# Performance work log

Measured on AMD Instinct MI355X. Metric: run time of the kernel, lower is better.

Reference implementation:

```python
import jax, jax.numpy as jnp
import numpy as np

DIM = 64
NUM_GRAPHS = 256  # B: number of graphs in the batch (static)


def setup_inputs() -> dict:
    key = jax.random.key(0)
    ks = jax.random.split(key, 16)
    N, E = 8000, 40000

    def p(k, shape, s=0.1):
        return jax.random.normal(k, shape, jnp.float32) * s

    return dict(
        x=jax.random.normal(ks[0], (N, 21), jnp.float32),
        edge_attr=jax.random.uniform(ks[1], (E, 16), jnp.float32),
        edge_index=jax.random.randint(ks[2], (2, E), 0, N, jnp.int32),
        batch=jnp.sort(jax.random.randint(ks[3], (N,), 0, NUM_GRAPHS, jnp.int32)),
        lin0_w=p(ks[4], (DIM, 21)), lin0_b=jnp.zeros((DIM,), jnp.float32),
        nn_w1=p(ks[5], (128, 16)), nn_b1=jnp.zeros((128,), jnp.float32),
        nn_w2=p(ks[6], (DIM * DIM, 128), 0.02), nn_b2=jnp.zeros((DIM * DIM,), jnp.float32),
        conv_root=p(ks[7], (DIM, DIM)), conv_bias=jnp.zeros((DIM,), jnp.float32),
        gru_w_ih=p(ks[8], (3 * DIM, DIM)), gru_w_hh=p(ks[9], (3 * DIM, DIM)),
        gru_b_ih=jnp.zeros((3 * DIM,), jnp.float32), gru_b_hh=jnp.zeros((3 * DIM,), jnp.float32),
        lstm_w_ih=p(ks[10], (4 * DIM, 2 * DIM)), lstm_w_hh=p(ks[11], (4 * DIM, DIM)),
        lstm_b_ih=jnp.zeros((4 * DIM,), jnp.float32), lstm_b_hh=jnp.zeros((4 * DIM,), jnp.float32),
        lin1_w=p(ks[12], (DIM, 2 * DIM)), lin1_b=jnp.zeros((DIM,), jnp.float32),
        lin2_w=p(ks[13], (1, DIM)), lin2_b=jnp.zeros((1,), jnp.float32),
    )


def reference(x, edge_attr, edge_index, batch,
              lin0_w, lin0_b, nn_w1, nn_b1, nn_w2, nn_b2,
              conv_root, conv_bias, gru_w_ih, gru_w_hh, gru_b_ih, gru_b_hh,
              lstm_w_ih, lstm_w_hh, lstm_b_ih, lstm_b_hh,
              lin1_w, lin1_b, lin2_w, lin2_b):
    N = x.shape[0]
    src, dst = edge_index[0], edge_index[1]

    out = jax.nn.relu(x @ lin0_w.T + lin0_b)           # [N, 64]
    h = out

    # edge-conditioned weights (same every iteration): [E, 64, 64]
    e_h = jax.nn.relu(edge_attr @ nn_w1.T + nn_b1)
    w_e = (e_h @ nn_w2.T + nn_b2).reshape(-1, DIM, DIM)

    deg = jax.ops.segment_sum(jnp.ones_like(src, jnp.float32), dst, num_segments=N)
    deg = jnp.maximum(deg, 1.0)[:, None]

    for _ in range(3):
        # NNConv: gather + per-edge matmul + scatter-mean + root/bias
        msg = jnp.einsum('ei,eio->eo', out[src], w_e)  # [E, 64]
        agg = jax.ops.segment_sum(msg, dst, num_segments=N) / deg
        m = jax.nn.relu(agg + out @ conv_root + conv_bias)
        # GRU cell (seq_len = 1), torch gate order r, z, n
        gi = m @ gru_w_ih.T + gru_b_ih
        gh = h @ gru_w_hh.T + gru_b_hh
        ir, iz, i_n = jnp.split(gi, 3, axis=-1)
        hr, hz, h_n = jnp.split(gh, 3, axis=-1)
        r = jax.nn.sigmoid(ir + hr)
        z = jax.nn.sigmoid(iz + hz)
        n = jnp.tanh(i_n + r * h_n)
        h = (1.0 - z) * n + z * h
        out = h

    # Set2Set pooling, 3 processing steps
    B = NUM_GRAPHS
    q_star = jnp.zeros((B, 2 * DIM), x.dtype)
    hs = jnp.zeros((B, DIM), x.dtype)
    cs = jnp.zeros((B, DIM), x.dtype)
    for _ in range(3):
        gates = q_star @ lstm_w_ih.T + lstm_b_ih + hs @ lstm_w_hh.T + lstm_b_hh
        gi_, gf_, gg_, go_ = jnp.split(gates, 4, axis=-1)  # torch gate order i,f,g,o
        cs = jax.nn.sigmoid(gf_) * cs + jax.nn.sigmoid(gi_) * jnp.tanh(gg_)
        hs = jax.nn.sigmoid(go_) * jnp.tanh(cs)
        q = hs                                             # [B, 64]
        e = jnp.sum(out * q[batch], axis=-1)               # [N]
        mmax = jax.ops.segment_max(e, batch, num_segments=B)
        ex = jnp.exp(e - mmax[batch])
        s = jax.ops.segment_sum(ex, batch, num_segments=B)
        a = ex / s[batch]
        r_read = jax.ops.segment_sum(a[:, None] * out, batch, num_segments=B)
        q_star = jnp.concatenate([q, r_read], axis=-1)     # [B, 128]

    y = jax.nn.relu(q_star @ lin1_w.T + lin1_b)
    y = y @ lin2_w.T + lin2_b
    return y.reshape(-1)
```

## Files before the change

### kernel.cpp

```cpp
#include <hip/hip_runtime.h>
#include <math.h>

#define NN 8000
#define NE 40000
#define NGB 256
#define SK 8192
#define KSPLIT 16

typedef unsigned int u32;
typedef unsigned short u16;
typedef __attribute__((ext_vector_type(8))) short short8v;
typedef __attribute__((ext_vector_type(4))) float float4v;
typedef __attribute__((ext_vector_type(4))) unsigned int uint4v;

__device__ __forceinline__ float sigmoidf_(float x) { return 1.f / (1.f + expf(-x)); }

__device__ __forceinline__ u32 bf16_rne(float f) {
    u32 x = __builtin_bit_cast(u32, f);
    return (x + 0x7FFFu + ((x >> 16) & 1u)) >> 16;
}

__device__ __forceinline__ uint4v pack_bf8(const float v[8]) {
    u32 h[8];
#pragma unroll
    for (int j = 0; j < 8; ++j) h[j] = bf16_rne(v[j]);
    return (uint4v){ h[0] | (h[1] << 16), h[2] | (h[3] << 16),
                     h[4] | (h[5] << 16), h[6] | (h[7] << 16) };
}

__device__ __forceinline__ void pack8(const float* p, float scale, short8v& ah, short8v& al) {
    float v[8];
#pragma unroll
    for (int j = 0; j < 8; ++j) v[j] = p[j];
    u32 hu[8], lu[8];
#pragma unroll
    for (int j = 0; j < 8; ++j) {
        float s = v[j] * scale;
        hu[j] = bf16_rne(s);
        float fh = __builtin_bit_cast(float, hu[j] << 16);
        lu[j] = bf16_rne(s - fh);
    }
    uint4v hset = { hu[0] | (hu[1] << 16), hu[2] | (hu[3] << 16),
                    hu[4] | (hu[5] << 16), hu[6] | (hu[7] << 16) };
    uint4v lset = { lu[0] | (lu[1] << 16), lu[2] | (lu[3] << 16),
                    lu[4] | (lu[5] << 16), lu[6] | (lu[7] << 16) };
    ah = __builtin_bit_cast(short8v, hset);
    al = __builtin_bit_cast(short8v, lset);
}


__global__ void k_lin0(const float* __restrict__ x, const float* __restrict__ w,
                       const float* __restrict__ b, float* __restrict__ out) {
    __shared__ float xr[21];
    int n = blockIdx.x, t = threadIdx.x;
    if (t < 21) xr[t] = x[n * 21 + t];
    __syncthreads();
    float s = b[t];
#pragma unroll
    for (int c = 0; c < 21; ++c) s += xr[c] * w[t * 21 + c];
    out[n * 64 + t] = fmaxf(s, 0.f);
}

__global__ void k_eh(const float* __restrict__ ea, const float* __restrict__ w1,
                     const float* __restrict__ b1, float* __restrict__ e_h) {
    __shared__ float a[2][16];
    int t = threadIdx.x;
    int e0 = blockIdx.x * 2;
    if (t < 32) a[t >> 4][t & 15] = ea[(e0 + (t >> 4)) * 16 + (t & 15)];
    __syncthreads();
    int sub = t >> 7, j = t & 127;
    float s = b1[j];
#pragma unroll
    for (int c = 0; c < 16; ++c) s += a[sub][c] * w1[j * 16 + c];
    e_h[(size_t)(e0 + sub) * 128 + j] = fmaxf(s, 0.f);
}

__global__ void k_prep(const float* __restrict__ nn_w2, const float* __restrict__ conv_root,
                       const float* __restrict__ nn_b2, const float* __restrict__ w_ih,
                       const float* __restrict__ w_hh,
                       u16* __restrict__ Whi, u16* __restrict__ Wlo,
                       u16* __restrict__ Bmh, u16* __restrict__ Bml,
                       u16* __restrict__ Bih_h, u16* __restrict__ Bih_l,
                       u16* __restrict__ Bhh_h, u16* __restrict__ Bhh_l) {
    int idx = blockIdx.x * 256 + threadIdx.x;
    if (idx < 524288) {
        int o = idx >> 13, kap = idx & 8191;
        int i = kap >> 7, k = kap & 127;
        float v = nn_w2[(size_t)((i << 6) + o) * 128 + k];
        u32 h = bf16_rne(v);
        float fh = __builtin_bit_cast(float, h << 16);
        u32 l = bf16_rne(v - fh);
        int pos = ((kap >> 3) * 64 + o) * 8 + (kap & 7);
        Whi[pos] = (u16)h; Wlo[pos] = (u16)l;
    } else if (idx < 524288 + 8192) {
        int i2 = idx - 524288;
        int k = i2 >> 6, o = i2 & 63;
        float v = (k < 64) ? nn_b2[k * 64 + o] : conv_root[(k - 64) * 64 + o];
        u32 h = bf16_rne(v);
        float fh = __builtin_bit_cast(float, h << 16);
        u32 l = bf16_rne(v - fh);
        int pos = ((k >> 3) * 64 + o) * 8 + (k & 7);
        Bmh[pos] = (u16)h; Bml[pos] = (u16)l;
    } else if (idx < 524288 + 8192 + 24576) {
        int i3 = idx - 524288 - 8192;
        int half = i3 >= 12288;
        int i2 = i3 - half * 12288;
        int o = i2 % 192, k = i2 / 192;
        float v = half ? w_hh[o * 64 + k] : w_ih[o * 64 + k];
        u32 h = bf16_rne(v);
        float fh = __builtin_bit_cast(float, h << 16);
        u32 l = bf16_rne(v - fh);
        int pos = ((k >> 3) * 192 + o) * 8 + (k & 7);
        if (half) { Bhh_h[pos] = (u16)h; Bhh_l[pos] = (u16)l; }
        else      { Bih_h[pos] = (u16)h; Bih_l[pos] = (u16)l; }
    }
}

__global__ void k_deg(const int* __restrict__ dst, int* __restrict__ degi) {
    int e = blockIdx.x * blockDim.x + threadIdx.x;
    if (e < NE) atomicAdd(&degi[dst[e]], 1);
}

__global__ __launch_bounds__(1024) void k_scan(
    const int* __restrict__ degi, int* __restrict__ rowptr,
    int* __restrict__ cursor, float* __restrict__ degf) {
    __shared__ int tsum[1024];
    int t = threadIdx.x;
    int base = t * 8;
    int v[8];
    int s = 0;
#pragma unroll
    for (int j = 0; j < 8; ++j) {
        int i = base + j;
        v[j] = (i < NN) ? degi[i] : 0;
        s += v[j];
    }
    tsum[t] = s;
    __syncthreads();
    for (int off = 1; off < 1024; off <<= 1) {
        int add = (t >= off) ? tsum[t - off] : 0;
        __syncthreads();
        tsum[t] += add;
        __syncthreads();
    }
    int exc = (t == 0) ? 0 : tsum[t - 1];
#pragma unroll
    for (int j = 0; j < 8; ++j) {
        int i = base + j;
        if (i < NN) {
            rowptr[i] = exc; cursor[i] = exc;
            degf[i] = (float)(v[j] > 1 ? v[j] : 1);
            exc += v[j];
        }
    }
    if (t == 1023) rowptr[NN] = tsum[1023];
}

__global__ void k_fill(const int* __restrict__ dst, int* __restrict__ cursor,
                       int* __restrict__ elist) {
    int e = blockIdx.x * blockDim.x + threadIdx.x;
    if (e < NE) { int p = atomicAdd(&cursor[dst[e]], 1); elist[p] = e; }
}

__global__ void k_gstart(const int* __restrict__ batch, int* __restrict__ gstart) {
    int g = blockIdx.x * blockDim.x + threadIdx.x;
    if (g > NGB) return;
    int lo = 0, hi = NN;
    while (lo < hi) { int mid = (lo + hi) >> 1; if (batch[mid] < g) lo = mid + 1; else hi = mid; }
    gstart[g] = lo;
}

__global__ __launch_bounds__(256) void k_sbuild(
    const float* __restrict__ out, const float* __restrict__ e_h,
    const int* __restrict__ src, const int* __restrict__ rowptr,
    const int* __restrict__ elist, u16* __restrict__ S_bf,
    float* __restrict__ Osum, int base) {
    int t = threadIdx.x;
    int n = base + blockIdx.x;
    int ig = t >> 4;
    int k8 = t & 15;
    int lane = t & 63;
    float acc[4][8];
#pragma unroll
    for (int j = 0; j < 4; ++j)
#pragma unroll
        for (int c = 0; c < 8; ++c) acc[j][c] = 0.f;
    float osum = 0.f;
    int r0 = rowptr[n], r1 = rowptr[n + 1];
    const float4* out4 = (const float4*)out;
    const float4* eh4p = (const float4*)e_h;
    for (int idx = r0; idx < r1; ++idx) {
        int e = elist[idx];
        int sn = src[e];
        float4 e0 = eh4p[(size_t)e * 32 + k8 * 2];
        float4 e1 = eh4p[(size_t)e * 32 + k8 * 2 + 1];
        float ehv[8] = {e0.x, e0.y, e0.z, e0.w, e1.x, e1.y, e1.z, e1.w};
        float4 f = out4[sn * 16 + ig];
        float fv[4] = {f.x, f.y, f.z, f.w};
#pragma unroll
        for (int j = 0; j < 4; ++j)
#pragma unroll
            for (int c = 0; c < 8; ++c) acc[j][c] += fv[j] * ehv[c];
        if (t < 64) osum += out[(size_t)sn * 64 + lane];
    }
    uint4v* S4 = (uint4v*)S_bf;
    size_t rb = (size_t)blockIdx.x * (SK / 8);
#pragma unroll
    for (int j = 0; j < 4; ++j)
        S4[rb + (size_t)(ig * 4 + j) * 16 + k8] = pack_bf8(acc[j]);
    if (t < 64) Osum[(size_t)n * 64 + lane] = osum;
}

__global__ __launch_bounds__(64) void k_gemm(
    const u16* __restrict__ S_bf, const u16* __restrict__ Whi,
    const u16* __restrict__ Wlo, float* __restrict__ P, int base) {
    int lane = threadIdx.x;
    int lrow = lane & 15, lkg = lane >> 4;
    int m0 = blockIdx.x * 32;
    int ks = blockIdx.y;
    int kbase = ks * (SK / KSPLIT);
    float4v acc[2][4];
#pragma unroll
    for (int ms = 0; ms < 2; ++ms)
#pragma unroll
        for (int nt = 0; nt < 4; ++nt) acc[ms][nt] = (float4v){0.f, 0.f, 0.f, 0.f};
    const short8v* bhv = (const short8v*)Whi;
    const short8v* blv = (const short8v*)Wlo;
    const u16* ar0 = S_bf + (size_t)(m0 + lrow) * SK + kbase + lkg * 8;
    const u16* ar1 = ar0 + (size_t)16 * SK;
    int kc0 = (kbase >> 3) + lkg;

#pragma unroll 4
    for (int kk = 0; kk < SK / KSPLIT / 32; ++kk) {
        short8v ah0 = *(const short8v*)(ar0 + kk * 32);
        short8v ah1 = *(const short8v*)(ar1 + kk * 32);
        int bo = (kc0 + kk * 4) * 64 + lrow;
        short8v bh[4], bl[4];
#pragma unroll
        for (int nt = 0; nt < 4; ++nt) { bh[nt] = bhv[bo + nt * 16]; bl[nt] = blv[bo + nt * 16]; }
#pragma unroll
        for (int nt = 0; nt < 4; ++nt) {
            acc[0][nt] = __builtin_amdgcn_mfma_f32_16x16x32_bf16(ah0, bh[nt], acc[0][nt], 0, 0, 0);
            acc[0][nt] = __builtin_amdgcn_mfma_f32_16x16x32_bf16(ah0, bl[nt], acc[0][nt], 0, 0, 0);
            acc[1][nt] = __builtin_amdgcn_mfma_f32_16x16x32_bf16(ah1, bh[nt], acc[1][nt], 0, 0, 0);
            acc[1][nt] = __builtin_amdgcn_mfma_f32_16x16x32_bf16(ah1, bl[nt], acc[1][nt], 0, 0, 0);
        }
    }
    int gbase = base + m0;
#pragma unroll
    for (int ms = 0; ms < 2; ++ms)
#pragma unroll
        for (int nt = 0; nt < 4; ++nt)
#pragma unroll
            for (int jj = 0; jj < 4; ++jj) {
                int row = ms * 16 + lkg * 4 + jj;
                int o = nt * 16 + lrow;
                P[((size_t)ks * NN + gbase + row) * 64 + o] = acc[ms][nt][jj];
            }
}

__global__ __launch_bounds__(64) void k_node(
    float* __restrict__ out, const float* __restrict__ P,
    const float* __restrict__ Osum, const float* __restrict__ degf,
    const u16* __restrict__ Bmh, const u16* __restrict__ Bml,
    const u16* __restrict__ Bih_h, const u16* __restrict__ Bih_l,
    const u16* __restrict__ Bhh_h, const u16* __restrict__ Bhh_l,
    const float* __restrict__ conv_bias,
    const float* __restrict__ gb_ih, const float* __restrict__ gb_hh) {
    __shared__ float lds[16][68];
    int lane = threadIdx.x;
    int lrow = lane & 15, lkg = lane >> 4;
    int n0 = blockIdx.x * 16;
    int arow = n0 + lrow;

    {
        const float4* P4 = (const float4*)P;
        float4 ps[4];
#pragma unroll
        for (int c = 0; c < 4; ++c) ps[c] = make_float4(0.f, 0.f, 0.f, 0.f);
        for (int p = 0; p < KSPLIT; ++p) {
#pragma unroll
            for (int c = 0; c < 4; ++c) {
                float4 v = P4[(size_t)p * (NN * 16) + (size_t)arow * 16 + lkg * 4 + c];
                ps[c].x += v.x; ps[c].y += v.y; ps[c].z += v.z; ps[c].w += v.w;
            }
        }
#pragma unroll
        for (int c = 0; c < 4; ++c)
            *(float4*)&lds[lrow][lkg * 16 + c * 4] = ps[c];
    }
    __syncthreads();

    float invd = 1.f / degf[arow];
    float4v acc[4];
#pragma unroll
    for (int nt = 0; nt < 4; ++nt) acc[nt] = (float4v){0.f, 0.f, 0.f, 0.f};
    const short8v* bhv = (const short8v*)Bmh;
    const short8v* blv = (const short8v*)Bml;
#pragma unroll
    for (int s = 0; s < 4; ++s) {
        short8v ah, al;
        if (s < 2) pack8(&Osum[(size_t)arow * 64 + s * 32 + lkg * 8], invd, ah, al);
        else       pack8(&out[(size_t)arow * 64 + (s - 2) * 32 + lkg * 8], 1.f, ah, al);
        int kc = s * 4 + lkg;
#pragma unroll
        for (int nt = 0; nt < 4; ++nt) {
            short8v bh = bhv[kc * 64 + nt * 16 + lrow];
            short8v bl = blv[kc * 64 + nt * 16 + lrow];
            acc[nt] = __builtin_amdgcn_mfma_f32_16x16x32_bf16(ah, bh, acc[nt], 0, 0, 0);
            acc[nt] = __builtin_amdgcn_mfma_f32_16x16x32_bf16(al, bh, acc[nt], 0, 0, 0);
            acc[nt] = __builtin_amdgcn_mfma_f32_16x16x32_bf16(ah, bl, acc[nt], 0, 0, 0);
        }
    }
    float invd2[4];
#pragma unroll
    for (int jj = 0; jj < 4; ++jj) invd2[jj] = 1.f / degf[n0 + lkg * 4 + jj];
    float mval[4][4];
#pragma unroll
    for (int nt = 0; nt < 4; ++nt) {
        int o = nt * 16 + lrow;
        float cb = conv_bias[o];
#pragma unroll
        for (int jj = 0; jj < 4; ++jj)
            mval[nt][jj] = fmaxf(acc[nt][jj] + lds[lkg * 4 + jj][o] * invd2[jj] + cb, 0.f);
    }
    __syncthreads();
#pragma unroll
    for (int nt = 0; nt < 4; ++nt)
#pragma unroll
        for (int jj = 0; jj < 4; ++jj)
            lds[lkg * 4 + jj][nt * 16 + lrow] = mval[nt][jj];
    __syncthreads();

    float4v ai[12], ah_[12];
#pragma unroll
    for (int nt = 0; nt < 12; ++nt) { ai[nt] = (float4v){0.f, 0.f, 0.f, 0.f}; ah_[nt] = (float4v){0.f, 0.f, 0.f, 0.f}; }
    const short8v* bih_h = (const short8v*)Bih_h;
    const short8v* bih_l = (const short8v*)Bih_l;
    const short8v* bhh_h = (const short8v*)Bhh_h;
    const short8v* bhh_l = (const short8v*)Bhh_l;
#pragma unroll
    for (int s = 0; s < 2; ++s) {
        short8v mh, ml, hh, hl;
        pack8(&lds[lrow][s * 32 + lkg * 8], 1.f, mh, ml);
        pack8(&out[(size_t)arow * 64 + s * 32 + lkg * 8], 1.f, hh, hl);
        int kc = s * 4 + lkg;
#pragma unroll
        for (int nt = 0; nt < 12; ++nt) {
            int bo = kc * 192 + nt * 16 + lrow;
            short8v b1 = bih_h[bo], b2 = bih_l[bo];
            ai[nt] = __builtin_amdgcn_mfma_f32_16x16x32_bf16(mh, b1, ai[nt], 0, 0, 0);
            ai[nt] = __builtin_amdgcn_mfma_f32_16x16x32_bf16(ml, b1, ai[nt], 0, 0, 0);
            ai[nt] = __builtin_amdgcn_mfma_f32_16x16x32_bf16(mh, b2, ai[nt], 0, 0, 0);
            short8v b3 = bhh_h[bo], b4 = bhh_l[bo];
            ah_[nt] = __builtin_amdgcn_mfma_f32_16x16x32_bf16(hh, b3, ah_[nt], 0, 0, 0);
            ah_[nt] = __builtin_amdgcn_mfma_f32_16x16x32_bf16(hl, b3, ah_[nt], 0, 0, 0);
            ah_[nt] = __builtin_amdgcn_mfma_f32_16x16x32_bf16(hh, b4, ah_[nt], 0, 0, 0);
        }
    }
#pragma unroll
    for (int nt = 0; nt < 4; ++nt) {
        int o = nt * 16 + lrow;
        float bi0 = gb_ih[o], bi1 = gb_ih[64 + o], bi2 = gb_ih[128 + o];
        float bh0 = gb_hh[o], bh1 = gb_hh[64 + o], bh2 = gb_hh[128 + o];
#pragma unroll
        for (int jj = 0; jj < 4; ++jj) {
            int row = n0 + lkg * 4 + jj;
            float ir = ai[nt][jj] + bi0,  hr = ah_[nt][jj] + bh0;
            float iz = ai[nt + 4][jj] + bi1, hz = ah_[nt + 4][jj] + bh1;
            float in_ = ai[nt + 8][jj] + bi2, hn = ah_[nt + 8][jj] + bh2;
            float r = sigmoidf_(ir + hr);
            float z = sigmoidf_(iz + hz);
            float nv = tanhf(in_ + r * hn);
            float ho = out[(size_t)row * 64 + o];
            out[(size_t)row * 64 + o] = (1.f - z) * nv + z * ho;
        }
    }
}

__global__ __launch_bounds__(256) void k_s2s(
    const float* __restrict__ out, const int* __restrict__ gstart,
    const float* __restrict__ lw_ih, const float* __restrict__ lw_hh,
    const float* __restrict__ lb_ih, const float* __restrict__ lb_hh,
    const float* __restrict__ lin1_w, const float* __restrict__ lin1_b,
    const float* __restrict__ lin2_w, const float* __restrict__ lin2_b,
    float* __restrict__ yout) {
    __shared__ float qs[128], hsL[64], csL[64], gates[256];
    __shared__ float pv[384];
    __shared__ float red[4][64];
    __shared__ float sswv[4], mmaxw[4];
    int g = blockIdx.x, t = threadIdx.x, wv = t >> 6, lane = t & 63;
    int s0 = gstart[g], s1 = gstart[g + 1];
    if (t < 128) qs[t] = 0.f;
    if (t < 64) { hsL[t] = 0.f; csL[t] = 0.f; }
    __syncthreads();
    for (int st = 0; st < 3; ++st) {
        float s = lb_ih[t] + lb_hh[t];
        const float4* wi = (const float4*)&lw_ih[t * 128];
#pragma unroll
        for (int i = 0; i < 32; ++i) {
            float4 a = wi[i];
            s += qs[i * 4] * a.x + qs[i * 4 + 1] * a.y + qs[i * 4 + 2] * a.z + qs[i * 4 + 3] * a.w;
        }
        const float4* wh = (const float4*)&lw_hh[t * 64];
#pragma unroll
        for (int i = 0; i < 16; ++i) {
            float4 a = wh[i];
            s += hsL[i * 4] * a.x + hsL[i * 4 + 1] * a.y + hsL[i * 4 + 2] * a.z + hsL[i * 4 + 3] * a.w;
        }
        gates[t] = s;
        __syncthreads();
        if (t < 64) {
            float ig = sigmoidf_(gates[t]);
            float fg = sigmoidf_(gates[64 + t]);
            float gg = tanhf(gates[128 + t]);
            float og = sigmoidf_(gates[192 + t]);
            float c = fg * csL[t] + ig * gg;
            csL[t] = c;
            hsL[t] = og * tanhf(c);
        }
        __syncthreads();
        float wmax = -1e30f;
        for (int i = s0 + wv; i < s1; i += 4) {
            float p = out[(size_t)i * 64 + lane] * hsL[lane];
#pragma unroll
            for (int off = 32; off >= 1; off >>= 1) p += __shfl_xor(p, off);
            if (lane == 0) pv[i - s0] = p;
            wmax = fmaxf(wmax, p);
        }
        if (lane == 0) mmaxw[wv] = wmax;
        __syncthreads();
        float mmax = fmaxf(fmaxf(mmaxw[0], mmaxw[1]), fmaxf(mmaxw[2], mmaxw[3]));
        float ssum = 0.f, racc = 0.f;
        for (int i = s0 + wv; i < s1; i += 4) {
            float w = expf(pv[i - s0] - mmax);
            ssum += w;
            racc += w * out[(size_t)i * 64 + lane];
        }
        red[wv][lane] = racc;
        if (lane == 0) sswv[wv] = ssum;
        __syncthreads();
        if (t < 64) {
            float rt = red[0][t] + red[1][t] + red[2][t] + red[3][t];
            float stot = sswv[0] + sswv[1] + sswv[2] + sswv[3];
            qs[t] = hsL[t];
            qs[64 + t] = (s1 > s0) ? rt / stot : 0.f;
        }
        __syncthreads();
    }
    if (t < 64) {
        float s = lin1_b[t];
        const float4* w1 = (const float4*)&lin1_w[t * 128];
#pragma unroll
        for (int i = 0; i < 32; ++i) {
            float4 a = w1[i];
            s += qs[i * 4] * a.x + qs[i * 4 + 1] * a.y + qs[i * 4 + 2] * a.z + qs[i * 4 + 3] * a.w;
        }
        s = fmaxf(s, 0.f) * lin2_w[t];
#pragma unroll
        for (int off = 32; off >= 1; off >>= 1) s += __shfl_xor(s, off);
        if (t == 0) yout[g] = s + lin2_b[0];
    }
}

extern "C" void kernel_launch(void* const* d_in, const int* in_sizes, int n_in,
                              void* d_out, int out_size, void* d_ws, size_t ws_size,
                              hipStream_t stream) {
    (void)in_sizes; (void)n_in; (void)out_size;
    const float* x        = (const float*)d_in[0];
    const float* eattr    = (const float*)d_in[1];
    const int*   ei       = (const int*)d_in[2];
    const int*   batch    = (const int*)d_in[3];
    const float* lin0_w   = (const float*)d_in[4];
    const float* lin0_b   = (const float*)d_in[5];
    const float* nn_w1    = (const float*)d_in[6];
    const float* nn_b1    = (const float*)d_in[7];
    const float* nn_w2    = (const float*)d_in[8];
    const float* nn_b2    = (const float*)d_in[9];
    const float* conv_root= (const float*)d_in[10];
    const float* conv_bias= (const float*)d_in[11];
    const float* gw_ih    = (const float*)d_in[12];
    const float* gw_hh    = (const float*)d_in[13];
    const float* gb_ih    = (const float*)d_in[14];
    const float* gb_hh    = (const float*)d_in[15];
    const float* lw_ih    = (const float*)d_in[16];
    const float* lw_hh    = (const float*)d_in[17];
    const float* lb_ih    = (const float*)d_in[18];
    const float* lb_hh    = (const float*)d_in[19];
    const float* lin1_w   = (const float*)d_in[20];
    const float* lin1_b   = (const float*)d_in[21];
    const float* lin2_w   = (const float*)d_in[22];
    const float* lin2_b   = (const float*)d_in[23];
    const int* src = ei;
    const int* dst = ei + NE;

    char* w = (char*)d_ws;
    auto alloc = [&](size_t bytes) { char* p = w; w += (bytes + 255) & ~(size_t)255; return p; };
    float* out    = (float*)alloc((size_t)NN * 64 * 4);
    float* e_h    = (float*)alloc((size_t)NE * 128 * 4);
    u16*   Whi    = (u16*)alloc((size_t)64 * SK * 2);
    u16*   Wlo    = (u16*)alloc((size_t)64 * SK * 2);
    float* P      = (float*)alloc((size_t)KSPLIT * NN * 64 * 4);
    float* Osum   = (float*)alloc((size_t)NN * 64 * 4);
    u16*   Bmh    = (u16*)alloc((size_t)8192 * 2);
    u16*   Bml    = (u16*)alloc((size_t)8192 * 2);
    u16*   Bih_h  = (u16*)alloc((size_t)12288 * 2);
    u16*   Bih_l  = (u16*)alloc((size_t)12288 * 2);
    u16*   Bhh_h  = (u16*)alloc((size_t)12288 * 2);
    u16*   Bhh_l  = (u16*)alloc((size_t)12288 * 2);
    float* degf   = (float*)alloc((size_t)NN * 4);
    int*   degi   = (int*)alloc((size_t)NN * 4);
    int*   rowptr = (int*)alloc((size_t)(NN + 1) * 4);
    int*   cursor = (int*)alloc((size_t)(NN + 1) * 4);
    int*   elist  = (int*)alloc((size_t)NE * 4);
    int*   gstart = (int*)alloc((size_t)(NGB + 1) * 4);
    size_t used = (size_t)(w - (char*)d_ws);
    size_t avail = ws_size > used ? ws_size - used : 0;
    size_t maxrows = avail / ((size_t)SK * 2);
    int chunkN = maxrows > (size_t)NN ? NN : (int)maxrows;
    chunkN = (chunkN / 64) * 64;
    if (chunkN < 64) chunkN = 64;
    u16* S_bf = (u16*)w;

    hipMemsetAsync(degi, 0, (size_t)NN * 4, stream);

    k_lin0<<<NN, 64, 0, stream>>>(x, lin0_w, lin0_b, out);
    k_eh<<<NE / 2, 256, 0, stream>>>(eattr, nn_w1, nn_b1, e_h);
    k_prep<<<2176, 256, 0, stream>>>(nn_w2, conv_root, nn_b2, gw_ih, gw_hh,
                                     Whi, Wlo, Bmh, Bml, Bih_h, Bih_l, Bhh_h, Bhh_l);
    k_deg<<<(NE + 255) / 256, 256, 0, stream>>>(dst, degi);
    k_scan<<<1, 1024, 0, stream>>>(degi, rowptr, cursor, degf);
    k_fill<<<(NE + 255) / 256, 256, 0, stream>>>(dst, cursor, elist);
    k_gstart<<<5, 64, 0, stream>>>(batch, gstart);

    for (int it = 0; it < 3; ++it) {
        for (int cb = 0; cb < NN; cb += chunkN) {
            int cn = (NN - cb) < chunkN ? (NN - cb) : chunkN;
            k_sbuild<<<cn, 256, 0, stream>>>(out, e_h, src, rowptr, elist, S_bf, Osum, cb);
            k_gemm<<<dim3(cn / 32, KSPLIT), 64, 0, stream>>>(S_bf, Whi, Wlo, P, cb);
        }
        k_node<<<NN / 16, 64, 0, stream>>>(out, P, Osum, degf, Bmh, Bml,
                                           Bih_h, Bih_l, Bhh_h, Bhh_l,
                                           conv_bias, gb_ih, gb_hh);
    }

    k_s2s<<<NGB, 256, 0, stream>>>(out, gstart, lw_ih, lw_hh, lb_ih, lb_hh,
                                   lin1_w, lin1_b, lin2_w, lin2_b, (float*)d_out);
}
```

Before: 384.3 us.

## Fuse setup kernels and replace split-K partial buffer with atomic accumulation

Merges lin0, edge MLP, weight prep and graph-start search into one setup launch. Replaces the KSPLIT partial-product buffer and its reduction in k_node with float atomicAdd into a single Psum buffer, which k_sbuild zeroes. The GEMM blocks now hold two waves each. This is meant to cut launch count and the write and read traffic of the 16-way partial buffer, at the cost of atomic contention and non-deterministic summation order.

```diff
diff --git a/kernel.cpp b/kernel.cpp
--- a/kernel.cpp
+++ b/kernel.cpp
@@ -48,42 +48,44 @@
     al = __builtin_bit_cast(short8v, lset);
 }
 
-
-__global__ void k_lin0(const float* __restrict__ x, const float* __restrict__ w,
-                       const float* __restrict__ b, float* __restrict__ out) {
-    __shared__ float xr[21];
-    int n = blockIdx.x, t = threadIdx.x;
-    if (t < 21) xr[t] = x[n * 21 + t];
-    __syncthreads();
-    float s = b[t];
-#pragma unroll
-    for (int c = 0; c < 21; ++c) s += xr[c] * w[t * 21 + c];
-    out[n * 64 + t] = fmaxf(s, 0.f);
-}
-
-__global__ void k_eh(const float* __restrict__ ea, const float* __restrict__ w1,
-                     const float* __restrict__ b1, float* __restrict__ e_h) {
-    __shared__ float a[2][16];
-    int t = threadIdx.x;
-    int e0 = blockIdx.x * 2;
-    if (t < 32) a[t >> 4][t & 15] = ea[(e0 + (t >> 4)) * 16 + (t & 15)];
-    __syncthreads();
-    int sub = t >> 7, j = t & 127;
-    float s = b1[j];
-#pragma unroll
-    for (int c = 0; c < 16; ++c) s += a[sub][c] * w1[j * 16 + c];
-    e_h[(size_t)(e0 + sub) * 128 + j] = fmaxf(s, 0.f);
-}
-
-__global__ void k_prep(const float* __restrict__ nn_w2, const float* __restrict__ conv_root,
-                       const float* __restrict__ nn_b2, const float* __restrict__ w_ih,
-                       const float* __restrict__ w_hh,
-                       u16* __restrict__ Whi, u16* __restrict__ Wlo,
-                       u16* __restrict__ Bmh, u16* __restrict__ Bml,
-                       u16* __restrict__ Bih_h, u16* __restrict__ Bih_l,
-                       u16* __restrict__ Bhh_h, u16* __restrict__ Bhh_l) {
+#define SETUP_LIN0 (NN * 64)
+#define SETUP_EH   (NE * 128)
+#define SETUP_W2   (64 * SK)
+#define SETUP_MW   8192
+#define SETUP_GB   24576
+__global__ void k_setup(const float* __restrict__ x, const float* __restrict__ lin0_w,
+                        const float* __restrict__ lin0_b,
+                        const float* __restrict__ ea, const float* __restrict__ nn_w1,
+                        const float* __restrict__ nn_b1,
+                        const float* __restrict__ nn_w2, const float* __restrict__ conv_root,
+                        const float* __restrict__ nn_b2, const float* __restrict__ gw_ih,
+                        const float* __restrict__ gw_hh, const int* __restrict__ batch,
+                        float* __restrict__ out, float* __restrict__ e_h,
+                        u16* __restrict__ Whi, u16* __restrict__ Wlo,
+                        u16* __restrict__ Bmh, u16* __restrict__ Bml,
+                        u16* __restrict__ Bih_h, u16* __restrict__ Bih_l,
+                        u16* __restrict__ Bhh_h, u16* __restrict__ Bhh_l,
+                        int* __restrict__ gstart) {
     int idx = blockIdx.x * 256 + threadIdx.x;
-    if (idx < 524288) {
+    if (idx < SETUP_LIN0) {
+        int n = idx >> 6, o = idx & 63;
+        float s = lin0_b[o];
+#pragma unroll
+        for (int c = 0; c < 21; ++c) s += x[n * 21 + c] * lin0_w[o * 21 + c];
+        out[idx] = fmaxf(s, 0.f);
+        return;
+    }
+    idx -= SETUP_LIN0;
+    if (idx < SETUP_EH) {
+        int e = idx >> 7, j = idx & 127;
+        float s = nn_b1[j];
+#pragma unroll
+        for (int c = 0; c < 16; ++c) s += ea[e * 16 + c] * nn_w1[j * 16 + c];
+        e_h[idx] = fmaxf(s, 0.f);
+        return;
+    }
+    idx -= SETUP_EH;
+    if (idx < SETUP_W2) {
         int o = idx >> 13, kap = idx & 8191;
         int i = kap >> 7, k = kap & 127;
         float v = nn_w2[(size_t)((i << 6) + o) * 128 + k];
@@ -92,29 +94,42 @@
         u32 l = bf16_rne(v - fh);
         int pos = ((kap >> 3) * 64 + o) * 8 + (kap & 7);
         Whi[pos] = (u16)h; Wlo[pos] = (u16)l;
-    } else if (idx < 524288 + 8192) {
-        int i2 = idx - 524288;
-        int k = i2 >> 6, o = i2 & 63;
+        return;
+    }
+    idx -= SETUP_W2;
+    if (idx < SETUP_MW) {
+        int k = idx >> 6, o = idx & 63;
         float v = (k < 64) ? nn_b2[k * 64 + o] : conv_root[(k - 64) * 64 + o];
         u32 h = bf16_rne(v);
         float fh = __builtin_bit_cast(float, h << 16);
         u32 l = bf16_rne(v - fh);
         int pos = ((k >> 3) * 64 + o) * 8 + (k & 7);
         Bmh[pos] = (u16)h; Bml[pos] = (u16)l;
-    } else if (idx < 524288 + 8192 + 24576) {
-        int i3 = idx - 524288 - 8192;
-        int half = i3 >= 12288;
-        int i2 = i3 - half * 12288;
+        return;
+    }
+    idx -= SETUP_MW;
+    if (idx < SETUP_GB) {
+        int half = idx >= 12288;
+        int i2 = idx - half * 12288;
         int o = i2 % 192, k = i2 / 192;
-        float v = half ? w_hh[o * 64 + k] : w_ih[o * 64 + k];
+        float v = half ? gw_hh[o * 64 + k] : gw_ih[o * 64 + k];
         u32 h = bf16_rne(v);
         float fh = __builtin_bit_cast(float, h << 16);
         u32 l = bf16_rne(v - fh);
         int pos = ((k >> 3) * 192 + o) * 8 + (k & 7);
         if (half) { Bhh_h[pos] = (u16)h; Bhh_l[pos] = (u16)l; }
         else      { Bih_h[pos] = (u16)h; Bih_l[pos] = (u16)l; }
-    }
-}
+        return;
+    }
+    idx -= SETUP_GB;
+    if (idx <= NGB) {
+        int g = idx;
+        int lo = 0, hi = NN;
+        while (lo < hi) { int mid = (lo + hi) >> 1; if (batch[mid] < g) lo = mid + 1; else hi = mid; }
+        gstart[g] = lo;
+    }
+}
+#define SETUP_TOTAL (SETUP_LIN0 + SETUP_EH + SETUP_W2 + SETUP_MW + SETUP_GB + NGB + 1)
 
 __global__ void k_deg(const int* __restrict__ dst, int* __restrict__ degi) {
     int e = blockIdx.x * blockDim.x + threadIdx.x;
@@ -162,19 +177,11 @@
     if (e < NE) { int p = atomicAdd(&cursor[dst[e]], 1); elist[p] = e; }
 }
 
-__global__ void k_gstart(const int* __restrict__ batch, int* __restrict__ gstart) {
-    int g = blockIdx.x * blockDim.x + threadIdx.x;
-    if (g > NGB) return;
-    int lo = 0, hi = NN;
-    while (lo < hi) { int mid = (lo + hi) >> 1; if (batch[mid] < g) lo = mid + 1; else hi = mid; }
-    gstart[g] = lo;
-}
-
 __global__ __launch_bounds__(256) void k_sbuild(
     const float* __restrict__ out, const float* __restrict__ e_h,
     const int* __restrict__ src, const int* __restrict__ rowptr,
     const int* __restrict__ elist, u16* __restrict__ S_bf,
-    float* __restrict__ Osum, int base) {
+    float* __restrict__ Osum, float* __restrict__ Psum, int base) {
     int t = threadIdx.x;
     int n = base + blockIdx.x;
     int ig = t >> 4;
@@ -208,15 +215,19 @@
 #pragma unroll
     for (int j = 0; j < 4; ++j)
         S4[rb + (size_t)(ig * 4 + j) * 16 + k8] = pack_bf8(acc[j]);
-    if (t < 64) Osum[(size_t)n * 64 + lane] = osum;
-}
-
-__global__ __launch_bounds__(64) void k_gemm(
+    if (t < 64) {
+        Osum[(size_t)n * 64 + lane] = osum;
+        Psum[(size_t)n * 64 + lane] = 0.f;
+    }
+}
+
+__global__ __launch_bounds__(128) void k_gemm(
     const u16* __restrict__ S_bf, const u16* __restrict__ Whi,
-    const u16* __restrict__ Wlo, float* __restrict__ P, int base) {
-    int lane = threadIdx.x;
+    const u16* __restrict__ Wlo, float* __restrict__ Psum, int base) {
+    int t = threadIdx.x;
+    int wv = t >> 6, lane = t & 63;
     int lrow = lane & 15, lkg = lane >> 4;
-    int m0 = blockIdx.x * 32;
+    int m0 = blockIdx.x * 64 + wv * 32;
     int ks = blockIdx.y;
     int kbase = ks * (SK / KSPLIT);
     float4v acc[2][4];
@@ -255,12 +266,12 @@
             for (int jj = 0; jj < 4; ++jj) {
                 int row = ms * 16 + lkg * 4 + jj;
                 int o = nt * 16 + lrow;
-                P[((size_t)ks * NN + gbase + row) * 64 + o] = acc[ms][nt][jj];
+                atomicAdd(&Psum[(size_t)(gbase + row) * 64 + o], acc[ms][nt][jj]);
             }
 }
 
 __global__ __launch_bounds__(64) void k_node(
-    float* __restrict__ out, const float* __restrict__ P,
+    float* __restrict__ out, const float* __restrict__ Psum,
     const float* __restrict__ Osum, const float* __restrict__ degf,
     const u16* __restrict__ Bmh, const u16* __restrict__ Bml,
     const u16* __restrict__ Bih_h, const u16* __restrict__ Bih_l,
@@ -273,24 +284,6 @@
     int n0 = blockIdx.x * 16;
     int arow = n0 + lrow;
 
-    {
-        const float4* P4 = (const float4*)P;
-        float4 ps[4];
-#pragma unroll
-        for (int c = 0; c < 4; ++c) ps[c] = make_float4(0.f, 0.f, 0.f, 0.f);
-        for (int p = 0; p < KSPLIT; ++p) {
-#pragma unroll
-            for (int c = 0; c < 4; ++c) {
-                float4 v = P4[(size_t)p * (NN * 16) + (size_t)arow * 16 + lkg * 4 + c];
-                ps[c].x += v.x; ps[c].y += v.y; ps[c].z += v.z; ps[c].w += v.w;
-            }
-        }
-#pragma unroll
-        for (int c = 0; c < 4; ++c)
-            *(float4*)&lds[lrow][lkg * 16 + c * 4] = ps[c];
-    }
-    __syncthreads();
-
     float invd = 1.f / degf[arow];
     float4v acc[4];
 #pragma unroll
@@ -315,21 +308,17 @@
     float invd2[4];
 #pragma unroll
     for (int jj = 0; jj < 4; ++jj) invd2[jj] = 1.f / degf[n0 + lkg * 4 + jj];
-    float mval[4][4];
 #pragma unroll
     for (int nt = 0; nt < 4; ++nt) {
         int o = nt * 16 + lrow;
         float cb = conv_bias[o];
 #pragma unroll
-        for (int jj = 0; jj < 4; ++jj)
-            mval[nt][jj] = fmaxf(acc[nt][jj] + lds[lkg * 4 + jj][o] * invd2[jj] + cb, 0.f);
-    }
-    __syncthreads();
-#pragma unroll
-    for (int nt = 0; nt < 4; ++nt)
-#pragma unroll
-        for (int jj = 0; jj < 4; ++jj)
-            lds[lkg * 4 + jj][nt * 16 + lrow] = mval[nt][jj];
+        for (int jj = 0; jj < 4; ++jj) {
+            int row = n0 + lkg * 4 + jj;
+            lds[lkg * 4 + jj][o] =
+                fmaxf(acc[nt][jj] + Psum[(size_t)row * 64 + o] * invd2[jj] + cb, 0.f);
+        }
+    }
     __syncthreads();
 
     float4v ai[12], ah_[12];
@@ -500,7 +489,7 @@
     float* e_h    = (float*)alloc((size_t)NE * 128 * 4);
     u16*   Whi    = (u16*)alloc((size_t)64 * SK * 2);
     u16*   Wlo    = (u16*)alloc((size_t)64 * SK * 2);
-    float* P      = (float*)alloc((size_t)KSPLIT * NN * 64 * 4);
+    float* Psum   = (float*)alloc((size_t)NN * 64 * 4);
     float* Osum   = (float*)alloc((size_t)NN * 64 * 4);
     u16*   Bmh    = (u16*)alloc((size_t)8192 * 2);
     u16*   Bml    = (u16*)alloc((size_t)8192 * 2);
@@ -524,22 +513,21 @@
 
     hipMemsetAsync(degi, 0, (size_t)NN * 4, stream);
 
-    k_lin0<<<NN, 64, 0, stream>>>(x, lin0_w, lin0_b, out);
-    k_eh<<<NE / 2, 256, 0, stream>>>(eattr, nn_w1, nn_b1, e_h);
-    k_prep<<<2176, 256, 0, stream>>>(nn_w2, conv_root, nn_b2, gw_ih, gw_hh,
-                                     Whi, Wlo, Bmh, Bml, Bih_h, Bih_l, Bhh_h, Bhh_l);
+    k_setup<<<(SETUP_TOTAL + 255) / 256, 256, 0, stream>>>(
+        x, lin0_w, lin0_b, eattr, nn_w1, nn_b1, nn_w2, conv_root, nn_b2,
+        gw_ih, gw_hh, batch, out, e_h, Whi, Wlo, Bmh, Bml,
+        Bih_h, Bih_l, Bhh_h, Bhh_l, gstart);
     k_deg<<<(NE + 255) / 256, 256, 0, stream>>>(dst, degi);
     k_scan<<<1, 1024, 0, stream>>>(degi, rowptr, cursor, degf);
     k_fill<<<(NE + 255) / 256, 256, 0, stream>>>(dst, cursor, elist);
-    k_gstart<<<5, 64, 0, stream>>>(batch, gstart);
 
     for (int it = 0; it < 3; ++it) {
         for (int cb = 0; cb < NN; cb += chunkN) {
             int cn = (NN - cb) < chunkN ? (NN - cb) : chunkN;
-            k_sbuild<<<cn, 256, 0, stream>>>(out, e_h, src, rowptr, elist, S_bf, Osum, cb);
-            k_gemm<<<dim3(cn / 32, KSPLIT), 64, 0, stream>>>(S_bf, Whi, Wlo, P, cb);
-        }
-        k_node<<<NN / 16, 64, 0, stream>>>(out, P, Osum, degf, Bmh, Bml,
+            k_sbuild<<<cn, 256, 0, stream>>>(out, e_h, src, rowptr, elist, S_bf, Osum, Psum, cb);
+            k_gemm<<<dim3(cn / 64, KSPLIT), 128, 0, stream>>>(S_bf, Whi, Wlo, Psum, cb);
+        }
+        k_node<<<NN / 16, 64, 0, stream>>>(out, Psum, Osum, degf, Bmh, Bml,
                                            Bih_h, Bih_l, Bhh_h, Bhh_l,
                                            conv_bias, gb_ih, gb_hh);
     }
```

Result: slower. 411.6 us (+7.1%).
